# Performance work log

Hardware: AMD Instinct MI355X
Metric: run time of the kernel (lower is better)

## Reference

```python
import jax, jax.numpy as jnp
import numpy as np

N_NODES = 100000
N_EDGES = 640000
HIDDEN = 128


def setup_inputs() -> dict:
    key = jax.random.key(0)
    k1, k2, k3, k4 = jax.random.split(key, 4)
    node_hidden = jax.random.normal(k1, (N_NODES, HIDDEN), dtype=jnp.float32)
    edge_hidden = jax.random.normal(k2, (N_EDGES, HIDDEN), dtype=jnp.float32)
    edge_index = jax.random.randint(k3, (2, N_EDGES), 0, N_NODES, dtype=jnp.int64)
    # Linear(3*HIDDEN, 1): store weight as [3d, 1] (transposed torch layout)
    W = jax.random.normal(k4, (3 * HIDDEN, 1), dtype=jnp.float32) / np.sqrt(3 * HIDDEN)
    b = jnp.zeros((1,), dtype=jnp.float32)
    return {"node_hidden": node_hidden, "edge_hidden": edge_hidden,
            "edge_index": edge_index, "W": W, "b": b}


def reference(node_hidden, edge_hidden, edge_index, W, b):
    src = node_hidden[edge_index[0]]          # [E, d] gather
    dst = node_hidden[edge_index[1]]          # [E, d] gather
    d = edge_hidden.shape[-1]
    # concat([edge_hidden, src, dst]) @ W + b, without materializing [E, 3d]
    W_e, W_s, W_d = W[:d], W[d:2 * d], W[2 * d:]
    out = edge_hidden @ W_e + src @ W_s + dst @ W_d + b  # [E, 1]
    return out
```

## Files before the change

### kernel.cpp

```cpp
#include <hip/hip_runtime.h>

#define HIDDEN 128

typedef float v4f __attribute__((ext_vector_type(4)));

__device__ __forceinline__ float dot4(const v4f a, const v4f b) {
    return a.x * b.x + a.y * b.y + a.z * b.z + a.w * b.w;
}

__global__ __launch_bounds__(256)
void node_dots_kernel(const float* __restrict__ node_hidden,
                      const float* __restrict__ W,
                      float* __restrict__ ns,
                      float* __restrict__ nd,
                      int n_nodes) {
    const int tid  = blockIdx.x * blockDim.x + threadIdx.x;
    const int node = tid >> 5;
    const int lane = tid & 31;
    if (node >= n_nodes) return;

    const v4f v  = reinterpret_cast<const v4f*>(node_hidden + (size_t)node * HIDDEN)[lane];
    const v4f ws = reinterpret_cast<const v4f*>(W + HIDDEN)[lane];
    const v4f wd = reinterpret_cast<const v4f*>(W + 2 * HIDDEN)[lane];

    float as = dot4(v, ws);
    float ad = dot4(v, wd);

    #pragma unroll
    for (int off = 16; off > 0; off >>= 1) {
        as += __shfl_down(as, off, 32);
        ad += __shfl_down(ad, off, 32);
    }
    if (lane == 0) {
        ns[node] = as;
        nd[node] = ad;
    }
}

__global__ __launch_bounds__(256)
void edge_fused_kernel(const float* __restrict__ edge_hidden,
                       const int*   __restrict__ edge_index,
                       const float* __restrict__ W,
                       const float* __restrict__ b,
                       const float* __restrict__ ns,
                       const float* __restrict__ nd,
                       float* __restrict__ out,
                       int n_edges) {
    const int tid  = blockIdx.x * blockDim.x + threadIdx.x;
    const int grp  = tid >> 5;
    const int lane = tid & 31;
    const int e0   = grp * 4;
    if (e0 >= n_edges) return;

    float base = 0.0f;
    const int my_e = e0 + lane;
    if (lane < 4 && my_e < n_edges) {
        const int s = edge_index[my_e];
        const int d = edge_index[n_edges + my_e];
        base = ns[s] + nd[d] + b[0];
    }

    const v4f we = reinterpret_cast<const v4f*>(W)[lane];
    const v4f* r = reinterpret_cast<const v4f*>(edge_hidden) + (size_t)e0 * 32 + lane;
    const v4f x0 = r[0];
    const v4f x1 = r[32];
    const v4f x2 = r[64];
    const v4f x3 = r[96];

    float a0 = dot4(x0, we);
    float a1 = dot4(x1, we);
    float a2 = dot4(x2, we);
    float a3 = dot4(x3, we);

    #pragma unroll
    for (int off = 16; off > 0; off >>= 1) {
        a0 += __shfl_xor(a0, off, 32);
        a1 += __shfl_xor(a1, off, 32);
        a2 += __shfl_xor(a2, off, 32);
        a3 += __shfl_xor(a3, off, 32);
    }

    if (lane < 4 && my_e < n_edges) {
        const float a = (lane == 0) ? a0 : (lane == 1) ? a1 : (lane == 2) ? a2 : a3;
        out[my_e] = a + base;
    }
}

extern "C" void kernel_launch(void* const* d_in, const int* in_sizes, int n_in,
                              void* d_out, int out_size, void* d_ws, size_t ws_size,
                              hipStream_t stream) {
    const float* node_hidden = (const float*)d_in[0];
    const float* edge_hidden = (const float*)d_in[1];
    const int*   edge_index  = (const int*)d_in[2];
    const float* W           = (const float*)d_in[3];
    const float* b           = (const float*)d_in[4];
    float* out = (float*)d_out;

    const int n_nodes = in_sizes[0] / HIDDEN;
    const int n_edges = in_sizes[2] / 2;

    float* ns = (float*)d_ws;
    float* nd = ns + n_nodes;

    {
        const int threads = 256;
        const int blocks = (n_nodes * 32 + threads - 1) / threads;
        node_dots_kernel<<<blocks, threads, 0, stream>>>(node_hidden, W, ns, nd, n_nodes);
    }
    {
        const int threads = 256;
        const int groups  = (n_edges + 3) / 4;
        const int blocks  = (groups * 32 + threads - 1) / threads;
        edge_fused_kernel<<<blocks, threads, 0, stream>>>(edge_hidden, edge_index, W, b,
                                                          ns, nd, out, n_edges);
    }
}
```

Baseline: 70.60 us.

## Co-schedule node dots with edge streaming and defer gather-add to second pass

Merges the node-dot and edge-dot work into one launch partitioned by block index, so the node projections no longer have to finish before the large edge_hidden stream begins. The gather of node scores plus bias moves to a small second kernel that adds into the output. Node scores are stored interleaved as float2. This trades an extra read-modify-write of the output and a separate index/gather pass for removing the serialization between the two phases.

After: 78.18 us. 10.7% more time.

```diff
diff --git a/kernel.cpp b/kernel.cpp
--- a/kernel.cpp
+++ b/kernel.cpp
@@ -9,81 +9,78 @@
 }
 
 __global__ __launch_bounds__(256)
-void node_dots_kernel(const float* __restrict__ node_hidden,
-                      const float* __restrict__ W,
-                      float* __restrict__ ns,
-                      float* __restrict__ nd,
-                      int n_nodes) {
-    const int tid  = blockIdx.x * blockDim.x + threadIdx.x;
-    const int node = tid >> 5;
-    const int lane = tid & 31;
-    if (node >= n_nodes) return;
+void pass1_kernel(const float* __restrict__ node_hidden,
+                  const float* __restrict__ edge_hidden,
+                  const float* __restrict__ W,
+                  float2* __restrict__ nsd,
+                  float* __restrict__ out,
+                  int n_nodes, int n_edges, int edge_blocks) {
+    const int lane = threadIdx.x & 31;
 
-    const v4f v  = reinterpret_cast<const v4f*>(node_hidden + (size_t)node * HIDDEN)[lane];
-    const v4f ws = reinterpret_cast<const v4f*>(W + HIDDEN)[lane];
-    const v4f wd = reinterpret_cast<const v4f*>(W + 2 * HIDDEN)[lane];
+    if ((int)blockIdx.x < edge_blocks) {
+        const int tid = blockIdx.x * blockDim.x + threadIdx.x;
+        const int grp = tid >> 5;
+        const int e0  = grp * 4;
+        if (e0 >= n_edges) return;
 
-    float as = dot4(v, ws);
-    float ad = dot4(v, wd);
+        const v4f we = reinterpret_cast<const v4f*>(W)[lane];
+        const v4f* r = reinterpret_cast<const v4f*>(edge_hidden) + (size_t)e0 * 32 + lane;
+        const v4f x0 = r[0];
+        const v4f x1 = r[32];
+        const v4f x2 = r[64];
+        const v4f x3 = r[96];
 
-    #pragma unroll
-    for (int off = 16; off > 0; off >>= 1) {
-        as += __shfl_down(as, off, 32);
-        ad += __shfl_down(ad, off, 32);
-    }
-    if (lane == 0) {
-        ns[node] = as;
-        nd[node] = ad;
+        float a0 = dot4(x0, we);
+        float a1 = dot4(x1, we);
+        float a2 = dot4(x2, we);
+        float a3 = dot4(x3, we);
+
+        #pragma unroll
+        for (int off = 16; off > 0; off >>= 1) {
+            a0 += __shfl_xor(a0, off, 32);
+            a1 += __shfl_xor(a1, off, 32);
+            a2 += __shfl_xor(a2, off, 32);
+            a3 += __shfl_xor(a3, off, 32);
+        }
+
+        const int my_e = e0 + lane;
+        if (lane < 4 && my_e < n_edges) {
+            const float a = (lane == 0) ? a0 : (lane == 1) ? a1 : (lane == 2) ? a2 : a3;
+            out[my_e] = a;
+        }
+    } else {
+        const int tid  = (blockIdx.x - edge_blocks) * blockDim.x + threadIdx.x;
+        const int node = tid >> 5;
+        if (node >= n_nodes) return;
+
+        const v4f v  = reinterpret_cast<const v4f*>(node_hidden + (size_t)node * HIDDEN)[lane];
+        const v4f ws = reinterpret_cast<const v4f*>(W + HIDDEN)[lane];
+        const v4f wd = reinterpret_cast<const v4f*>(W + 2 * HIDDEN)[lane];
+
+        float as = dot4(v, ws);
+        float ad = dot4(v, wd);
+
+        #pragma unroll
+        for (int off = 16; off > 0; off >>= 1) {
+            as += __shfl_down(as, off, 32);
+            ad += __shfl_down(ad, off, 32);
+        }
+        if (lane == 0)
+            nsd[node] = make_float2(as, ad);
     }
 }
 
 __global__ __launch_bounds__(256)
-void edge_fused_kernel(const float* __restrict__ edge_hidden,
-                       const int*   __restrict__ edge_index,
-                       const float* __restrict__ W,
-                       const float* __restrict__ b,
-                       const float* __restrict__ ns,
-                       const float* __restrict__ nd,
-                       float* __restrict__ out,
-                       int n_edges) {
-    const int tid  = blockIdx.x * blockDim.x + threadIdx.x;
-    const int grp  = tid >> 5;
-    const int lane = tid & 31;
-    const int e0   = grp * 4;
-    if (e0 >= n_edges) return;
-
-    float base = 0.0f;
-    const int my_e = e0 + lane;
-    if (lane < 4 && my_e < n_edges) {
-        const int s = edge_index[my_e];
-        const int d = edge_index[n_edges + my_e];
-        base = ns[s] + nd[d] + b[0];
-    }
-
-    const v4f we = reinterpret_cast<const v4f*>(W)[lane];
-    const v4f* r = reinterpret_cast<const v4f*>(edge_hidden) + (size_t)e0 * 32 + lane;
-    const v4f x0 = r[0];
-    const v4f x1 = r[32];
-    const v4f x2 = r[64];
-    const v4f x3 = r[96];
-
-    float a0 = dot4(x0, we);
-    float a1 = dot4(x1, we);
-    float a2 = dot4(x2, we);
-    float a3 = dot4(x3, we);
-
-    #pragma unroll
-    for (int off = 16; off > 0; off >>= 1) {
-        a0 += __shfl_xor(a0, off, 32);
-        a1 += __shfl_xor(a1, off, 32);
-        a2 += __shfl_xor(a2, off, 32);
-        a3 += __shfl_xor(a3, off, 32);
-    }
-
-    if (lane < 4 && my_e < n_edges) {
-        const float a = (lane == 0) ? a0 : (lane == 1) ? a1 : (lane == 2) ? a2 : a3;
-        out[my_e] = a + base;
-    }
+void add_base_kernel(const int* __restrict__ edge_index,
+                     const float2* __restrict__ nsd,
+                     const float* __restrict__ b,
+                     float* __restrict__ out,
+                     int n_edges) {
+    const int e = blockIdx.x * blockDim.x + threadIdx.x;
+    if (e >= n_edges) return;
+    const int s = edge_index[e];
+    const int d = edge_index[n_edges + e];
+    out[e] += nsd[s].x + nsd[d].y + b[0];
 }
 
 extern "C" void kernel_launch(void* const* d_in, const int* in_sizes, int n_in,
@@ -99,19 +96,19 @@
     const int n_nodes = in_sizes[0] / HIDDEN;
     const int n_edges = in_sizes[2] / 2;
 
-    float* ns = (float*)d_ws;
-    float* nd = ns + n_nodes;
+    float2* nsd = (float2*)d_ws;
 
     {
         const int threads = 256;
-        const int blocks = (n_nodes * 32 + threads - 1) / threads;
-        node_dots_kernel<<<blocks, threads, 0, stream>>>(node_hidden, W, ns, nd, n_nodes);
+        const int edge_groups = (n_edges + 3) / 4;
+        const int edge_blocks = (edge_groups * 32 + threads - 1) / threads;
+        const int node_blocks = (n_nodes * 32 + threads - 1) / threads;
+        pass1_kernel<<<edge_blocks + node_blocks, threads, 0, stream>>>(
+            node_hidden, edge_hidden, W, nsd, out, n_nodes, n_edges, edge_blocks);
     }
     {
         const int threads = 256;
-        const int groups  = (n_edges + 3) / 4;
-        const int blocks  = (groups * 32 + threads - 1) / threads;
-        edge_fused_kernel<<<blocks, threads, 0, stream>>>(edge_hidden, edge_index, W, b,
-                                                          ns, nd, out, n_edges);
+        const int blocks = (n_edges + threads - 1) / threads;
+        add_base_kernel<<<blocks, threads, 0, stream>>>(edge_index, nsd, b, out, n_edges);
     }
 }
```

## Batch node dots, interleave ns/nd, widen edge groups with nontemporal loads

Applied to the files above, without the earlier changes.

The node kernel now has each 32-lane group process four nodes and write the source and destination scalars together as one float2 array. The edge kernel has each group handle eight edges with nontemporal streaming loads, so more memory requests are in flight per wave. The interleaved layout lets the two random gathers per edge hit one array. Handling the remainder needs a separate scalar tail path, and the node kernel's per-wave work grows from one node to four, so it launches fewer blocks.

Measured after the change: 65.05 us. -7.9%, faster.

```diff
diff --git a/kernel.cpp b/kernel.cpp
--- a/kernel.cpp
+++ b/kernel.cpp
@@ -11,29 +11,58 @@
 __global__ __launch_bounds__(256)
 void node_dots_kernel(const float* __restrict__ node_hidden,
                       const float* __restrict__ W,
-                      float* __restrict__ ns,
-                      float* __restrict__ nd,
+                      float2* __restrict__ nsd,
                       int n_nodes) {
     const int tid  = blockIdx.x * blockDim.x + threadIdx.x;
-    const int node = tid >> 5;
+    const int grp  = tid >> 5;
     const int lane = tid & 31;
-    if (node >= n_nodes) return;
+    const int n0   = grp * 4;
+    if (n0 >= n_nodes) return;
 
-    const v4f v  = reinterpret_cast<const v4f*>(node_hidden + (size_t)node * HIDDEN)[lane];
     const v4f ws = reinterpret_cast<const v4f*>(W + HIDDEN)[lane];
     const v4f wd = reinterpret_cast<const v4f*>(W + 2 * HIDDEN)[lane];
 
-    float as = dot4(v, ws);
-    float ad = dot4(v, wd);
+    if (n0 + 4 <= n_nodes) {
+        const v4f* r = reinterpret_cast<const v4f*>(node_hidden) + (size_t)n0 * 32 + lane;
+        const v4f x0 = __builtin_nontemporal_load(r + 0);
+        const v4f x1 = __builtin_nontemporal_load(r + 32);
+        const v4f x2 = __builtin_nontemporal_load(r + 64);
+        const v4f x3 = __builtin_nontemporal_load(r + 96);
 
-    #pragma unroll
-    for (int off = 16; off > 0; off >>= 1) {
-        as += __shfl_down(as, off, 32);
-        ad += __shfl_down(ad, off, 32);
-    }
-    if (lane == 0) {
-        ns[node] = as;
-        nd[node] = ad;
+        float as0 = dot4(x0, ws), ad0 = dot4(x0, wd);
+        float as1 = dot4(x1, ws), ad1 = dot4(x1, wd);
+        float as2 = dot4(x2, ws), ad2 = dot4(x2, wd);
+        float as3 = dot4(x3, ws), ad3 = dot4(x3, wd);
+
+        #pragma unroll
+        for (int off = 16; off > 0; off >>= 1) {
+            as0 += __shfl_xor(as0, off, 32);
+            ad0 += __shfl_xor(ad0, off, 32);
+            as1 += __shfl_xor(as1, off, 32);
+            ad1 += __shfl_xor(ad1, off, 32);
+            as2 += __shfl_xor(as2, off, 32);
+            ad2 += __shfl_xor(ad2, off, 32);
+            as3 += __shfl_xor(as3, off, 32);
+            ad3 += __shfl_xor(ad3, off, 32);
+        }
+
+        if (lane < 4) {
+            const float as = (lane == 0) ? as0 : (lane == 1) ? as1 : (lane == 2) ? as2 : as3;
+            const float ad = (lane == 0) ? ad0 : (lane == 1) ? ad1 : (lane == 2) ? ad2 : ad3;
+            nsd[n0 + lane] = make_float2(as, ad);
+        }
+    } else {
+        for (int n = n0; n < n_nodes; ++n) {
+            const v4f v = reinterpret_cast<const v4f*>(node_hidden + (size_t)n * HIDDEN)[lane];
+            float as = dot4(v, ws);
+            float ad = dot4(v, wd);
+            #pragma unroll
+            for (int off = 16; off > 0; off >>= 1) {
+                as += __shfl_down(as, off, 32);
+                ad += __shfl_down(ad, off, 32);
+            }
+            if (lane == 0) nsd[n] = make_float2(as, ad);
+        }
     }
 }
 
@@ -42,47 +71,76 @@
                        const int*   __restrict__ edge_index,
                        const float* __restrict__ W,
                        const float* __restrict__ b,
-                       const float* __restrict__ ns,
-                       const float* __restrict__ nd,
+                       const float2* __restrict__ nsd,
                        float* __restrict__ out,
                        int n_edges) {
     const int tid  = blockIdx.x * blockDim.x + threadIdx.x;
     const int grp  = tid >> 5;
     const int lane = tid & 31;
-    const int e0   = grp * 4;
+    const int e0   = grp * 8;
     if (e0 >= n_edges) return;
 
     float base = 0.0f;
     const int my_e = e0 + lane;
-    if (lane < 4 && my_e < n_edges) {
+    if (lane < 8 && my_e < n_edges) {
         const int s = edge_index[my_e];
         const int d = edge_index[n_edges + my_e];
-        base = ns[s] + nd[d] + b[0];
+        base = nsd[s].x + nsd[d].y + b[0];
     }
 
     const v4f we = reinterpret_cast<const v4f*>(W)[lane];
-    const v4f* r = reinterpret_cast<const v4f*>(edge_hidden) + (size_t)e0 * 32 + lane;
-    const v4f x0 = r[0];
-    const v4f x1 = r[32];
-    const v4f x2 = r[64];
-    const v4f x3 = r[96];
 
-    float a0 = dot4(x0, we);
-    float a1 = dot4(x1, we);
-    float a2 = dot4(x2, we);
-    float a3 = dot4(x3, we);
+    if (e0 + 8 <= n_edges) {
+        const v4f* r = reinterpret_cast<const v4f*>(edge_hidden) + (size_t)e0 * 32 + lane;
+        const v4f x0 = __builtin_nontemporal_load(r + 0);
+        const v4f x1 = __builtin_nontemporal_load(r + 32);
+        const v4f x2 = __builtin_nontemporal_load(r + 64);
+        const v4f x3 = __builtin_nontemporal_load(r + 96);
+        const v4f x4 = __builtin_nontemporal_load(r + 128);
+        const v4f x5 = __builtin_nontemporal_load(r + 160);
+        const v4f x6 = __builtin_nontemporal_load(r + 192);
+        const v4f x7 = __builtin_nontemporal_load(r + 224);
 
-    #pragma unroll
-    for (int off = 16; off > 0; off >>= 1) {
-        a0 += __shfl_xor(a0, off, 32);
-        a1 += __shfl_xor(a1, off, 32);
-        a2 += __shfl_xor(a2, off, 32);
-        a3 += __shfl_xor(a3, off, 32);
-    }
+        float a0 = dot4(x0, we);
+        float a1 = dot4(x1, we);
+        float a2 = dot4(x2, we);
+        float a3 = dot4(x3, we);
+        float a4 = dot4(x4, we);
+        float a5 = dot4(x5, we);
+        float a6 = dot4(x6, we);
+        float a7 = dot4(x7, we);
 
-    if (lane < 4 && my_e < n_edges) {
-        const float a = (lane == 0) ? a0 : (lane == 1) ? a1 : (lane == 2) ? a2 : a3;
-        out[my_e] = a + base;
+        #pragma unroll
+        for (int off = 16; off > 0; off >>= 1) {
+            a0 += __shfl_xor(a0, off, 32);
+            a1 += __shfl_xor(a1, off, 32);
+            a2 += __shfl_xor(a2, off, 32);
+            a3 += __shfl_xor(a3, off, 32);
+            a4 += __shfl_xor(a4, off, 32);
+            a5 += __shfl_xor(a5, off, 32);
+            a6 += __shfl_xor(a6, off, 32);
+            a7 += __shfl_xor(a7, off, 32);
+        }
+
+        if (lane < 8) {
+            const float a = (lane == 0) ? a0 : (lane == 1) ? a1 : (lane == 2) ? a2 :
+                            (lane == 3) ? a3 : (lane == 4) ? a4 : (lane == 5) ? a5 :
+                            (lane == 6) ? a6 : a7;
+            out[my_e] = a + base;
+        }
+    } else {
+        for (int e = e0; e < n_edges; ++e) {
+            const v4f x = reinterpret_cast<const v4f*>(edge_hidden + (size_t)e * HIDDEN)[lane];
+            float a = dot4(x, we);
+            #pragma unroll
+            for (int off = 16; off > 0; off >>= 1)
+                a += __shfl_down(a, off, 32);
+            if (lane == 0) {
+                const int s = edge_index[e];
+                const int d = edge_index[n_edges + e];
+                out[e] = a + nsd[s].x + nsd[d].y + b[0];
+            }
+        }
     }
 }
 
@@ -99,19 +157,19 @@
     const int n_nodes = in_sizes[0] / HIDDEN;
     const int n_edges = in_sizes[2] / 2;
 
-    float* ns = (float*)d_ws;
-    float* nd = ns + n_nodes;
+    float2* nsd = (float2*)d_ws;
 
     {
         const int threads = 256;
-        const int blocks = (n_nodes * 32 + threads - 1) / threads;
-        node_dots_kernel<<<blocks, threads, 0, stream>>>(node_hidden, W, ns, nd, n_nodes);
+        const int groups  = (n_nodes + 3) / 4;
+        const int blocks  = (groups * 32 + threads - 1) / threads;
+        node_dots_kernel<<<blocks, threads, 0, stream>>>(node_hidden, W, nsd, n_nodes);
     }
     {
         const int threads = 256;
-        const int groups  = (n_edges + 3) / 4;
+        const int groups  = (n_edges + 7) / 8;
         const int blocks  = (groups * 32 + threads - 1) / threads;
         edge_fused_kernel<<<blocks, threads, 0, stream>>>(edge_hidden, edge_index, W, b,
-                                                          ns, nd, out, n_edges);
+                                                          nsd, out, n_edges);
     }
 }
```
